# Kernel optimization log

Hardware: AMD Instinct MI355X
Metric: run time of the kernel (lower is better)

The kernel has to match this reference:

```python
import jax, jax.numpy as jnp
import numpy as np

N, E, P = 20000, 320000, 100000
TC, HID, H, OUT, PH = 256, 64, 4, 256, 512


def gat_conv(x, src, dst, n, W, a_src, a_dst, b):
    # PyG GATConv (eval, dropout=0): per-head linear, LeakyReLU(0.2) attention,
    # scatter-softmax over incoming edges, scatter-add aggregation, concat heads + bias.
    Hh, C = a_src.shape
    h = (x @ W).reshape(n, Hh, C)
    alpha_src = (h * a_src).sum(-1)  # [N, H]
    alpha_dst = (h * a_dst).sum(-1)  # [N, H]
    e = jax.nn.leaky_relu(alpha_src[src] + alpha_dst[dst], 0.2)  # [E, H]
    emax = jax.ops.segment_max(e, dst, num_segments=n)
    emax = jnp.where(jnp.isfinite(emax), emax, 0.0)
    p = jnp.exp(e - emax[dst])
    denom = jax.ops.segment_sum(p, dst, num_segments=n)
    alpha = p / jnp.maximum(denom[dst], 1e-16)  # [E, H]
    out = jax.ops.segment_sum(h[src] * alpha[:, :, None], dst, num_segments=n)  # [N, H, C]
    return out.reshape(n, Hh * C) + b


def setup_inputs() -> dict:
    key = jax.random.key(0)
    ks = jax.random.split(key, 24)
    s = 0.05
    inp = {
        "x": jax.random.normal(ks[0], (N, TC), jnp.float32),
        "edge_index": jax.random.randint(ks[1], (2, E), 0, N, jnp.int64),
        "u_nodes": jax.random.randint(ks[2], (P,), 0, N, jnp.int64),
        "v_nodes": jax.random.randint(ks[3], (P,), 0, N, jnp.int64),
        # GATConv 1: in=TC, out=HID per head, heads=H, concat
        "W1": jax.random.normal(ks[4], (TC, H * HID), jnp.float32) * s,
        "a1s": jax.random.normal(ks[5], (H, HID), jnp.float32) * s,
        "a1d": jax.random.normal(ks[6], (H, HID), jnp.float32) * s,
        "b1": jax.random.normal(ks[7], (H * HID,), jnp.float32) * s,
        # GATConv 2: in=H*HID, out=OUT, heads=1
        "W2": jax.random.normal(ks[8], (H * HID, OUT), jnp.float32) * s,
        "a2s": jax.random.normal(ks[9], (1, OUT), jnp.float32) * s,
        "a2d": jax.random.normal(ks[10], (1, OUT), jnp.float32) * s,
        "b2": jax.random.normal(ks[11], (OUT,), jnp.float32) * s,
        # gate MLP: (TC+OUT) -> (TC+OUT)//2 -> 1, Sigmoid
        "gw1": jax.random.normal(ks[12], (TC + OUT, (TC + OUT) // 2), jnp.float32) * s,
        "gb1": jax.random.normal(ks[13], ((TC + OUT) // 2,), jnp.float32) * s,
        "gw2": jax.random.normal(ks[14], ((TC + OUT) // 2, 1), jnp.float32) * s,
        "gb2": jax.random.normal(ks[15], (1,), jnp.float32) * s,
        # predictor: 2*OUT -> PH -> 1 (dropout is identity in eval)
        "pw1": jax.random.normal(ks[16], (2 * OUT, PH), jnp.float32) * s,
        "pb1": jax.random.normal(ks[17], (PH,), jnp.float32) * s,
        "pw2": jax.random.normal(ks[18], (PH, 1), jnp.float32) * s,
        "pb2": jax.random.normal(ks[19], (1,), jnp.float32) * s,
    }
    return inp


def reference(x, edge_index, u_nodes, v_nodes, W1, a1s, a1d, b1, W2, a2s, a2d, b2,
              gw1, gb1, gw2, gb2, pw1, pb1, pw2, pb2):
    n = x.shape[0]
    loops = jnp.arange(n, dtype=edge_index.dtype)
    src = jnp.concatenate([edge_index[0], loops])  # PyG GATConv adds self-loops
    dst = jnp.concatenate([edge_index[1], loops])
    h = jax.nn.elu(gat_conv(x, src, dst, n, W1, a1s, a1d, b1))
    h_graph = gat_conv(h, src, dst, n, W2, a2s, a2d, b2)
    gate_in = jnp.concatenate([x, h_graph], axis=-1)
    g = jax.nn.sigmoid(jax.nn.relu(gate_in @ gw1 + gb1) @ gw2 + gb2)  # [N,1]
    h_final = (1.0 - g) * x + g * h_graph
    pair = jnp.concatenate([h_final[u_nodes], h_final[v_nodes]], axis=-1)  # [P, 2*OUT]
    out = jax.nn.relu(pair @ pw1 + pb1) @ pw2 + pb2
    return out.squeeze(-1)
```

## Files before the change

### kernel.cpp

```cpp
#include <hip/hip_runtime.h>
#include <math.h>

#define N_NODES 20000
#define N_EDGES 320000
#define EPRIME  (N_EDGES + N_NODES)
#define NP      100000

typedef __bf16 bf16x8 __attribute__((ext_vector_type(8)));
typedef float  f32x4  __attribute__((ext_vector_type(4)));

__device__ __forceinline__ float b2f(unsigned short u) {
    union { float f; unsigned int v; } x; x.v = ((unsigned int)u) << 16; return x.f;
}
__device__ __forceinline__ unsigned short f2b(float f) {
    union { float f; unsigned int v; } x; x.f = f;
    unsigned int r = (x.v + 0x7fffu + ((x.v >> 16) & 1u)) >> 16;
    return (unsigned short)r;
}
__device__ __forceinline__ float lrelu02(float v) { return v > 0.0f ? v : 0.2f * v; }

__device__ __forceinline__ void gload16(const void* g, void* l) {
    __builtin_amdgcn_global_load_lds(
        (const __attribute__((address_space(1))) void*)g,
        (__attribute__((address_space(3))) void*)l, 16, 0, 0);
}

template<int ASRC, int EPI>
__global__ __launch_bounds__(256) void mgemm_k(
    const unsigned short* __restrict__ A0, const unsigned short* __restrict__ A1,
    const int* __restrict__ idxU, const int* __restrict__ idxV,
    const unsigned short* __restrict__ BT,
    const float* __restrict__ bias, const float* __restrict__ w2,
    unsigned short* __restrict__ Cb, float* __restrict__ outp,
    int M, int K, int Nn)
{
    __shared__ unsigned short As[2][4096];
    __shared__ unsigned short Bs[2][4096];

    const int tid = threadIdx.x;
    const int wave = tid >> 6, lane = tid & 63;
    const int row0 = blockIdx.x * 128, col0 = blockIdx.y * 128;
    const int ksub = (((lane & 3) ^ ((lane >> 3) & 3)) * 8);

    const unsigned short* aL[2];
    const unsigned short* aH[2];
    const unsigned short* bP[2];
    #pragma unroll
    for (int j = 0; j < 2; ++j) {
        const int r = j * 64 + wave * 16 + (lane >> 2);
        int ar = row0 + r; if (ar > M - 1) ar = M - 1;
        if (ASRC == 0)      { aL[j] = A0 + (long)ar * K;  aH[j] = aL[j]; }
        else if (ASRC == 1) { aL[j] = A0 + (long)ar * 256; aH[j] = A1 + (long)ar * 256; }
        else { const int u = idxU[ar], v = idxV[ar];
               aL[j] = A0 + (long)u * 256;  aH[j] = A0 + (long)v * 256; }
        bP[j] = BT + (long)(col0 + r) * K;
    }

    const int wm = wave >> 1, wn = wave & 1;
    const int lrow = lane & 15;
    const int lks = ((((lane >> 4) ^ ((lane >> 1) & 3)) & 3) * 8);

    f32x4 acc[4][4] = {};

    const int nT = K >> 5;
    int buf = 0;

    auto stage = [&](int bi, int t) {
        const int k0 = t << 5;
        #pragma unroll
        for (int j = 0; j < 2; ++j) {
            const unsigned short* ga;
            if (ASRC == 0) ga = aL[j] + k0 + ksub;
            else ga = (k0 < 256) ? (aL[j] + k0 + ksub) : (aH[j] + (k0 - 256) + ksub);
            const int ci = j * 256 + wave * 64 + lane;
            gload16(ga, &As[bi][ci * 8]);
            gload16(bP[j] + k0 + ksub, &Bs[bi][ci * 8]);
        }
    };

    stage(0, 0);
    __syncthreads();
    for (int t = 0; t < nT; ++t) {
        if (t + 1 < nT) stage(buf ^ 1, t + 1);
        bf16x8 a[4], b[4];
        #pragma unroll
        for (int i = 0; i < 4; ++i)
            a[i] = *(const bf16x8*)&As[buf][(wm * 64 + i * 16 + lrow) * 32 + lks];
        #pragma unroll
        for (int j = 0; j < 4; ++j)
            b[j] = *(const bf16x8*)&Bs[buf][(wn * 64 + j * 16 + lrow) * 32 + lks];
        #pragma unroll
        for (int i = 0; i < 4; ++i)
            #pragma unroll
            for (int j = 0; j < 4; ++j)
                acc[i][j] = __builtin_amdgcn_mfma_f32_16x16x32_bf16(a[i], b[j], acc[i][j], 0, 0, 0);
        __syncthreads();
        buf ^= 1;
    }

    if constexpr (EPI == 0 || EPI == 1) {
        #pragma unroll
        for (int i = 0; i < 4; ++i) {
            #pragma unroll
            for (int p = 0; p < 4; ++p) {
                const int row = row0 + wm * 64 + i * 16 + (lane >> 4) * 4 + p;
                if (row < M) {
                    #pragma unroll
                    for (int j = 0; j < 4; ++j) {
                        const int col = col0 + wn * 64 + j * 16 + (lane & 15);
                        float v = acc[i][j][p];
                        if (EPI == 1) { v += bias[col]; v = v > 0.f ? v : 0.f; }
                        Cb[(long)row * Nn + col] = f2b(v);
                    }
                }
            }
        }
    } else {
        float s[4][4];
        #pragma unroll
        for (int i = 0; i < 4; ++i) {
            #pragma unroll
            for (int p = 0; p < 4; ++p) {
                float t = 0.f;
                #pragma unroll
                for (int j = 0; j < 4; ++j) {
                    const int col = col0 + wn * 64 + j * 16 + (lane & 15);
                    float v = acc[i][j][p] + bias[col];
                    v = v > 0.f ? v : 0.f;
                    t += v * w2[col];
                }
                s[i][p] = t;
            }
        }
        #pragma unroll
        for (int off = 1; off < 16; off <<= 1) {
            #pragma unroll
            for (int i = 0; i < 4; ++i)
                #pragma unroll
                for (int p = 0; p < 4; ++p)
                    s[i][p] += __shfl_xor(s[i][p], off);
        }
        if ((lane & 15) == 0) {
            #pragma unroll
            for (int i = 0; i < 4; ++i)
                #pragma unroll
                for (int p = 0; p < 4; ++p) {
                    const int row = row0 + wm * 64 + i * 16 + (lane >> 4) * 4 + p;
                    if (row < M) atomicAdd(outp + row, s[i][p]);
                }
        }
    }
}

__global__ __launch_bounds__(256) void pair_k(
    const unsigned short* __restrict__ Z, const int* __restrict__ un,
    const int* __restrict__ vn, const float* __restrict__ pb1,
    const float* __restrict__ pw2, const float* __restrict__ pb2,
    float* __restrict__ out)
{
    const int wv = threadIdx.x >> 6, lane = threadIdx.x & 63;
    const int p = blockIdx.x * 4 + wv;
    if (p >= NP) return;
    const int u = un[p], v = vn[p];
    const int c0 = lane * 8;
    const uint4 zu = *(const uint4*)&Z[(long)u * 1024 + c0];
    const uint4 zv = *(const uint4*)&Z[(long)v * 1024 + 512 + c0];
    const float4 b1a = *(const float4*)&pb1[c0];
    const float4 b1b = *(const float4*)&pb1[c0 + 4];
    const float4 w2a = *(const float4*)&pw2[c0];
    const float4 w2b = *(const float4*)&pw2[c0 + 4];

    float zt[8], zb[8];
    zt[0] = b2f(zu.x & 0xffff); zt[1] = b2f(zu.x >> 16);
    zt[2] = b2f(zu.y & 0xffff); zt[3] = b2f(zu.y >> 16);
    zt[4] = b2f(zu.z & 0xffff); zt[5] = b2f(zu.z >> 16);
    zt[6] = b2f(zu.w & 0xffff); zt[7] = b2f(zu.w >> 16);
    zb[0] = b2f(zv.x & 0xffff); zb[1] = b2f(zv.x >> 16);
    zb[2] = b2f(zv.y & 0xffff); zb[3] = b2f(zv.y >> 16);
    zb[4] = b2f(zv.z & 0xffff); zb[5] = b2f(zv.z >> 16);
    zb[6] = b2f(zv.w & 0xffff); zb[7] = b2f(zv.w >> 16);

    const float bb[8] = {b1a.x, b1a.y, b1a.z, b1a.w, b1b.x, b1b.y, b1b.z, b1b.w};
    const float ww[8] = {w2a.x, w2a.y, w2a.z, w2a.w, w2b.x, w2b.y, w2b.z, w2b.w};
    float s = 0.f;
    #pragma unroll
    for (int q = 0; q < 8; ++q) {
        float t = zt[q] + zb[q] + bb[q];
        t = t > 0.f ? t : 0.f;
        s = fmaf(t, ww[q], s);
    }
    #pragma unroll
    for (int off = 1; off < 64; off <<= 1) s += __shfl_xor(s, off);
    if (lane == 0) out[p] = s + pb2[0];
}

__global__ __launch_bounds__(256) void castx_k(const float* __restrict__ x,
                                               unsigned short* __restrict__ xb)
{
    const int id = blockIdx.x * 256 + threadIdx.x;
    const float4 v = ((const float4*)x)[id];
    ushort4 o;
    o.x = f2b(v.x); o.y = f2b(v.y); o.z = f2b(v.z); o.w = f2b(v.w);
    ((ushort4*)xb)[id] = o;
}

__global__ __launch_bounds__(256) void tr_k(const float* __restrict__ B,
                                            unsigned short* __restrict__ BT,
                                            int K, int N)
{
    const int id = blockIdx.x * 256 + threadIdx.x;
    const int k = id / N, n = id % N;
    BT[(long)n * K + k] = f2b(B[id]);
}

__global__ __launch_bounds__(256) void tr2_k(const float* __restrict__ pw1,
                                             unsigned short* __restrict__ BT2)
{
    const int id = blockIdx.x * 256 + threadIdx.x;
    const int r = id >> 9, c = id & 511;
    const int j = (r < 256) ? c : (512 + c);
    const int k = (r < 256) ? r : (r - 256);
    BT2[j * 256 + k] = f2b(pw1[id]);
}

__global__ __launch_bounds__(256) void alpha1_k(
    const unsigned short* __restrict__ h1, const float* __restrict__ a1s,
    const float* __restrict__ a1d, float* __restrict__ as1, float* __restrict__ ad1)
{
    const int wid = threadIdx.x >> 6;
    const int lane = threadIdx.x & 63;
    const int n = blockIdx.x * 4 + wid;
    if (n >= N_NODES) return;
    float ps[4], pd[4];
    #pragma unroll
    for (int h = 0; h < 4; ++h) {
        const float hv = b2f(h1[(long)n * 256 + h * 64 + lane]);
        ps[h] = hv * a1s[h * 64 + lane];
        pd[h] = hv * a1d[h * 64 + lane];
    }
    #pragma unroll
    for (int off = 32; off > 0; off >>= 1) {
        #pragma unroll
        for (int h = 0; h < 4; ++h) {
            ps[h] += __shfl_xor(ps[h], off);
            pd[h] += __shfl_xor(pd[h], off);
        }
    }
    if (lane == 0) {
        #pragma unroll
        for (int h = 0; h < 4; ++h) {
            as1[n * 4 + h] = ps[h];
            ad1[n * 4 + h] = pd[h];
        }
    }
}

__global__ __launch_bounds__(256) void alpha2_k(
    const unsigned short* __restrict__ h2, const float* __restrict__ a2s,
    const float* __restrict__ a2d, float* __restrict__ as2, float* __restrict__ ad2)
{
    const int wid = threadIdx.x >> 6;
    const int lane = threadIdx.x & 63;
    const int n = blockIdx.x * 4 + wid;
    if (n >= N_NODES) return;
    float ps = 0.f, pd = 0.f;
    #pragma unroll
    for (int q = 0; q < 4; ++q) {
        const float hv = b2f(h2[(long)n * 256 + q * 64 + lane]);
        ps += hv * a2s[q * 64 + lane];
        pd += hv * a2d[q * 64 + lane];
    }
    #pragma unroll
    for (int off = 32; off > 0; off >>= 1) {
        ps += __shfl_xor(ps, off);
        pd += __shfl_xor(pd, off);
    }
    if (lane == 0) { as2[n] = ps; ad2[n] = pd; }
}

__global__ __launch_bounds__(256) void deg_init_k(int* __restrict__ deg)
{
    const int i = blockIdx.x * 256 + threadIdx.x;
    if (i < N_NODES) deg[i] = 1;
}

__global__ __launch_bounds__(256) void deg_count_k(const int* __restrict__ ei, int* __restrict__ deg)
{
    const int e = blockIdx.x * 256 + threadIdx.x;
    if (e < N_EDGES) atomicAdd(&deg[ei[N_EDGES + e]], 1);
}

__global__ __launch_bounds__(1024) void scan_k(const int* __restrict__ deg,
                                               int* __restrict__ indptr,
                                               int* __restrict__ pos)
{
    __shared__ int sums[1024];
    const int tid = threadIdx.x;
    const int CH = 20;
    const int start = tid * CH;
    const int end = min(start + CH, N_NODES);
    int s = 0;
    for (int i = start; i < end; ++i) s += deg[i];
    sums[tid] = s;
    __syncthreads();
    for (int off = 1; off < 1024; off <<= 1) {
        const int v = sums[tid];
        const int add = (tid >= off) ? sums[tid - off] : 0;
        __syncthreads();
        sums[tid] = v + add;
        __syncthreads();
    }
    int pre = sums[tid] - s;
    for (int i = start; i < end; ++i) {
        indptr[i] = pre;
        pos[i] = pre;
        pre += deg[i];
    }
    if (tid == 1023) indptr[N_NODES] = sums[1023];
}

__global__ __launch_bounds__(256) void fill_k(const int* __restrict__ ei,
                                              int* __restrict__ pos, int* __restrict__ csr)
{
    const int i = blockIdx.x * 256 + threadIdx.x;
    if (i < N_EDGES) {
        const int s = ei[i], d = ei[N_EDGES + i];
        const int p = atomicAdd(&pos[d], 1);
        csr[p] = s;
    } else if (i < EPRIME) {
        const int n = i - N_EDGES;
        const int p = atomicAdd(&pos[n], 1);
        csr[p] = n;
    }
}

__global__ __launch_bounds__(256) void agg1_k(
    const unsigned short* __restrict__ h1, const float* __restrict__ as1,
    const float* __restrict__ ad1, const int* __restrict__ indptr,
    const int* __restrict__ csr, const float* __restrict__ b1,
    unsigned short* __restrict__ out)
{
    __shared__ int   ssrc[4][64];
    __shared__ float sp[4][64 * 4];
    const int wv = threadIdx.x >> 6, lane = threadIdx.x & 63;
    const int n = blockIdx.x * 4 + wv;
    if (n >= N_NODES) return;

    const int beg = indptr[n], end = indptr[n + 1];
    const float4 ad = ((const float4*)ad1)[n];
    const int c0 = lane * 4;
    const int hd = lane >> 4;

    float acc[4] = {0.f, 0.f, 0.f, 0.f};
    float psum[4] = {0.f, 0.f, 0.f, 0.f};

    for (int base = beg; base < end; base += 64) {
        const int cnt = min(64, end - base);
        if (lane < cnt) {
            const int s = csr[base + lane];
            const float4 av = ((const float4*)as1)[s];
            float4 p;
            p.x = __expf(lrelu02(av.x + ad.x));
            p.y = __expf(lrelu02(av.y + ad.y));
            p.z = __expf(lrelu02(av.z + ad.z));
            p.w = __expf(lrelu02(av.w + ad.w));
            ssrc[wv][lane] = s;
            *(float4*)&sp[wv][lane * 4] = p;
            psum[0] += p.x; psum[1] += p.y; psum[2] += p.z; psum[3] += p.w;
        }
        asm volatile("s_waitcnt lgkmcnt(0)" ::: "memory");
        __builtin_amdgcn_sched_barrier(0);
        for (int e = 0; e < cnt; ++e) {
            const int s = ssrc[wv][e];
            const float w = sp[wv][e * 4 + hd];
            const ushort4 hv = *(const ushort4*)&h1[(long)s * 256 + c0];
            acc[0] = fmaf(w, b2f(hv.x), acc[0]);
            acc[1] = fmaf(w, b2f(hv.y), acc[1]);
            acc[2] = fmaf(w, b2f(hv.z), acc[2]);
            acc[3] = fmaf(w, b2f(hv.w), acc[3]);
        }
        __builtin_amdgcn_sched_barrier(0);
        __builtin_amdgcn_wave_barrier();
    }

    #pragma unroll
    for (int off = 1; off < 64; off <<= 1) {
        #pragma unroll
        for (int h = 0; h < 4; ++h) psum[h] += __shfl_xor(psum[h], off);
    }
    const float invd = 1.0f / psum[hd];

    ushort4 o;
    float v;
    v = acc[0] * invd + b1[c0 + 0]; o.x = f2b(v > 0.f ? v : (__expf(v) - 1.0f));
    v = acc[1] * invd + b1[c0 + 1]; o.y = f2b(v > 0.f ? v : (__expf(v) - 1.0f));
    v = acc[2] * invd + b1[c0 + 2]; o.z = f2b(v > 0.f ? v : (__expf(v) - 1.0f));
    v = acc[3] * invd + b1[c0 + 3]; o.w = f2b(v > 0.f ? v : (__expf(v) - 1.0f));
    *(ushort4*)&out[(long)n * 256 + c0] = o;
}

__global__ __launch_bounds__(256) void agg2_k(
    const unsigned short* __restrict__ h2, const float* __restrict__ as2,
    const float* __restrict__ ad2, const int* __restrict__ indptr,
    const int* __restrict__ csr, const float* __restrict__ b2,
    unsigned short* __restrict__ outb)
{
    __shared__ int   ssrc[4][64];
    __shared__ float sp[4][64];
    const int wv = threadIdx.x >> 6, lane = threadIdx.x & 63;
    const int n = blockIdx.x * 4 + wv;
    if (n >= N_NODES) return;

    const int beg = indptr[n], end = indptr[n + 1];
    const float adv = ad2[n];
    const int c0 = lane * 4;

    float acc[4] = {0.f, 0.f, 0.f, 0.f};
    float psum = 0.f;

    for (int base = beg; base < end; base += 64) {
        const int cnt = min(64, end - base);
        if (lane < cnt) {
            const int s = csr[base + lane];
            const float p = __expf(lrelu02(as2[s] + adv));
            ssrc[wv][lane] = s;
            sp[wv][lane] = p;
            psum += p;
        }
        asm volatile("s_waitcnt lgkmcnt(0)" ::: "memory");
        __builtin_amdgcn_sched_barrier(0);
        for (int e = 0; e < cnt; ++e) {
            const int s = ssrc[wv][e];
            const float w = sp[wv][e];
            const ushort4 hv = *(const ushort4*)&h2[(long)s * 256 + c0];
            acc[0] = fmaf(w, b2f(hv.x), acc[0]);
            acc[1] = fmaf(w, b2f(hv.y), acc[1]);
            acc[2] = fmaf(w, b2f(hv.z), acc[2]);
            acc[3] = fmaf(w, b2f(hv.w), acc[3]);
        }
        __builtin_amdgcn_sched_barrier(0);
        __builtin_amdgcn_wave_barrier();
    }

    #pragma unroll
    for (int off = 1; off < 64; off <<= 1) psum += __shfl_xor(psum, off);
    const float invd = 1.0f / psum;

    ushort4 o;
    o.x = f2b(acc[0] * invd + b2[c0 + 0]);
    o.y = f2b(acc[1] * invd + b2[c0 + 1]);
    o.z = f2b(acc[2] * invd + b2[c0 + 2]);
    o.w = f2b(acc[3] * invd + b2[c0 + 3]);
    *(ushort4*)&outb[(long)n * 256 + c0] = o;
}

__global__ __launch_bounds__(256) void gatefin_k(
    const unsigned short* __restrict__ ghid, const float* __restrict__ gw2,
    const float* __restrict__ gb2, const float* __restrict__ x,
    const unsigned short* __restrict__ hgb, unsigned short* __restrict__ hfb)
{
    const int wid = threadIdx.x >> 6;
    const int lane = threadIdx.x & 63;
    const int n = blockIdx.x * 4 + wid;
    if (n >= N_NODES) return;
    float s = 0.f;
    #pragma unroll
    for (int q = 0; q < 4; ++q)
        s += b2f(ghid[(long)n * 256 + q * 64 + lane]) * gw2[q * 64 + lane];
    #pragma unroll
    for (int off = 32; off > 0; off >>= 1) s += __shfl_xor(s, off);
    const float g = 1.0f / (1.0f + __expf(-(s + gb2[0])));
    #pragma unroll
    for (int q = 0; q < 4; ++q) {
        const int c = q * 64 + lane;
        const float xv = x[(long)n * 256 + c];
        const float hv = b2f(hgb[(long)n * 256 + c]);
        hfb[(long)n * 256 + c] = f2b((1.0f - g) * xv + g * hv);
    }
}

__global__ __launch_bounds__(256) void outinit_k(float* __restrict__ out, const float* __restrict__ pb2)
{
    const int p = blockIdx.x * 256 + threadIdx.x;
    if (p < NP) out[p] = pb2[0];
}

extern "C" void kernel_launch(void* const* d_in, const int* in_sizes, int n_in,
                              void* d_out, int out_size, void* d_ws, size_t ws_size,
                              hipStream_t stream)
{
    const float* x   = (const float*)d_in[0];
    const int*   ei  = (const int*)d_in[1];
    const int*   un  = (const int*)d_in[2];
    const int*   vn  = (const int*)d_in[3];
    const float* W1  = (const float*)d_in[4];
    const float* a1s = (const float*)d_in[5];
    const float* a1d = (const float*)d_in[6];
    const float* b1  = (const float*)d_in[7];
    const float* W2  = (const float*)d_in[8];
    const float* a2s = (const float*)d_in[9];
    const float* a2d = (const float*)d_in[10];
    const float* b2  = (const float*)d_in[11];
    const float* gw1 = (const float*)d_in[12];
    const float* gb1 = (const float*)d_in[13];
    const float* gw2 = (const float*)d_in[14];
    const float* gb2 = (const float*)d_in[15];
    const float* pw1 = (const float*)d_in[16];
    const float* pb1 = (const float*)d_in[17];
    const float* pw2 = (const float*)d_in[18];
    const float* pb2 = (const float*)d_in[19];
    float* out = (float*)d_out;

    dim3 b256(256);

    if (ws_size >= 58720256u) {
        unsigned short* Z     = (unsigned short*)d_ws;
        unsigned short* bufHb = Z;
        unsigned short* hgb   = Z + 5120000;
        unsigned short* xb    = Z + 10240000;
        unsigned short* hfb   = Z + 20480000;
        unsigned short* W1t   = hfb + 5120000;
        unsigned short* W2t   = W1t + 65536;
        unsigned short* gw1t  = W2t + 65536;
        unsigned short* pw1t2 = gw1t + 131072;
        float* as1v = (float*)(pw1t2 + 262144);
        float* ad1v = as1v + 80000;
        float* as2v = ad1v + 80000;
        float* ad2v = as2v + 20000;
        int* deg    = (int*)(ad2v + 20000);
        int* indptr = deg + 20000;
        int* pos    = indptr + 20032;
        int* csr    = pos + 20000;

        castx_k<<<5000, b256, 0, stream>>>(x, xb);
        tr_k<<<65536 / 256, b256, 0, stream>>>(W1, W1t, 256, 256);
        tr_k<<<65536 / 256, b256, 0, stream>>>(W2, W2t, 256, 256);
        tr_k<<<131072 / 256, b256, 0, stream>>>(gw1, gw1t, 512, 256);
        tr2_k<<<262144 / 256, b256, 0, stream>>>(pw1, pw1t2);
        deg_init_k<<<(N_NODES + 255) / 256, b256, 0, stream>>>(deg);
        deg_count_k<<<(N_EDGES + 255) / 256, b256, 0, stream>>>(ei, deg);
        scan_k<<<1, 1024, 0, stream>>>(deg, indptr, pos);
        fill_k<<<(EPRIME + 255) / 256, b256, 0, stream>>>(ei, pos, csr);

        mgemm_k<0, 0><<<dim3(157, 2), b256, 0, stream>>>(
            xb, nullptr, nullptr, nullptr, W1t, nullptr, nullptr, bufHb, nullptr,
            N_NODES, 256, 256);
        alpha1_k<<<5000, b256, 0, stream>>>(bufHb, a1s, a1d, as1v, ad1v);
        agg1_k<<<5000, b256, 0, stream>>>(bufHb, as1v, ad1v, indptr, csr, b1, hfb);

        mgemm_k<0, 0><<<dim3(157, 2), b256, 0, stream>>>(
            hfb, nullptr, nullptr, nullptr, W2t, nullptr, nullptr, bufHb, nullptr,
            N_NODES, 256, 256);
        alpha2_k<<<5000, b256, 0, stream>>>(bufHb, a2s, a2d, as2v, ad2v);
        agg2_k<<<5000, b256, 0, stream>>>(bufHb, as2v, ad2v, indptr, csr, b2, hgb);

        mgemm_k<1, 1><<<dim3(157, 2), b256, 0, stream>>>(
            xb, hgb, nullptr, nullptr, gw1t, gb1, nullptr, bufHb, nullptr,
            N_NODES, 512, 256);
        gatefin_k<<<5000, b256, 0, stream>>>(bufHb, gw2, gb2, x, hgb, hfb);

        mgemm_k<0, 0><<<dim3(157, 8), b256, 0, stream>>>(
            hfb, nullptr, nullptr, nullptr, pw1t2, nullptr, nullptr, Z, nullptr,
            N_NODES, 256, 1024);

        pair_k<<<25000, b256, 0, stream>>>(Z, un, vn, pb1, pw2, pb2, out);
        return;
    }

    unsigned short* bufHb = (unsigned short*)d_ws;
    unsigned short* h1ab  = bufHb + 5120000;
    unsigned short* hgb   = h1ab + 5120000;
    unsigned short* xb    = hgb + 5120000;
    unsigned short* W1t   = xb + 5120000;
    unsigned short* W2t   = W1t + 65536;
    unsigned short* gw1t  = W2t + 65536;
    unsigned short* pw1t  = gw1t + 131072;
    float* as1v = (float*)(pw1t + 262144);
    float* ad1v = as1v + 80000;
    float* as2v = ad1v + 80000;
    float* ad2v = as2v + 20000;
    int* deg    = (int*)(ad2v + 20000);
    int* indptr = deg + 20000;
    int* pos    = indptr + 20032;
    int* csr    = pos + 20000;
    if (ws_size < 46u * 1024u * 1024u) return;

    castx_k<<<5000, b256, 0, stream>>>(x, xb);
    tr_k<<<65536 / 256, b256, 0, stream>>>(W1, W1t, 256, 256);
    tr_k<<<65536 / 256, b256, 0, stream>>>(W2, W2t, 256, 256);
    tr_k<<<131072 / 256, b256, 0, stream>>>(gw1, gw1t, 512, 256);
    tr_k<<<262144 / 256, b256, 0, stream>>>(pw1, pw1t, 512, 512);
    deg_init_k<<<(N_NODES + 255) / 256, b256, 0, stream>>>(deg);
    deg_count_k<<<(N_EDGES + 255) / 256, b256, 0, stream>>>(ei, deg);
    scan_k<<<1, 1024, 0, stream>>>(deg, indptr, pos);
    fill_k<<<(EPRIME + 255) / 256, b256, 0, stream>>>(ei, pos, csr);

    mgemm_k<0, 0><<<dim3(157, 2), b256, 0, stream>>>(
        xb, nullptr, nullptr, nullptr, W1t, nullptr, nullptr, bufHb, nullptr,
        N_NODES, 256, 256);
    alpha1_k<<<5000, b256, 0, stream>>>(bufHb, a1s, a1d, as1v, ad1v);
    agg1_k<<<5000, b256, 0, stream>>>(bufHb, as1v, ad1v, indptr, csr, b1, h1ab);

    mgemm_k<0, 0><<<dim3(157, 2), b256, 0, stream>>>(
        h1ab, nullptr, nullptr, nullptr, W2t, nullptr, nullptr, bufHb, nullptr,
        N_NODES, 256, 256);
    alpha2_k<<<5000, b256, 0, stream>>>(bufHb, a2s, a2d, as2v, ad2v);
    agg2_k<<<5000, b256, 0, stream>>>(bufHb, as2v, ad2v, indptr, csr, b2, hgb);

    mgemm_k<1, 1><<<dim3(157, 2), b256, 0, stream>>>(
        xb, hgb, nullptr, nullptr, gw1t, gb1, nullptr, bufHb, nullptr,
        N_NODES, 512, 256);
    gatefin_k<<<5000, b256, 0, stream>>>(bufHb, gw2, gb2, x, hgb, h1ab);

    outinit_k<<<(NP + 255) / 256, b256, 0, stream>>>(out, pb2);
    mgemm_k<2, 2><<<dim3(782, 4), b256, 0, stream>>>(
        h1ab, nullptr, un, vn, pw1t, pb1, pw2, nullptr, out,
        NP, 512, 512);
}
```

Before: 264.1 us.

## Merge prep kernels, shrink GEMM row tiles, fuse gate MLP output into GEMM epilogue

Replaces the cast, transpose and init launches with one combined prep kernel. Adds a BM template parameter so the N=20000 GEMMs use 64-row tiles, giving more blocks to fill the CUs. The gate MLP's second layer and sigmoid input are folded into the GEMM epilogue through atomic row reductions, which removes the bf16 hidden-buffer round trip. The predictor's first-layer bias is added in the Z GEMM epilogue instead of in pair_k. Smaller tiles reload B more often, and the atomics add contention.

New measurement: 257.1 us. -2.7%, faster.

```diff
diff --git a/kernel.cpp b/kernel.cpp
--- a/kernel.cpp
+++ b/kernel.cpp
@@ -25,7 +25,7 @@
         (__attribute__((address_space(3))) void*)l, 16, 0, 0);
 }
 
-template<int ASRC, int EPI>
+template<int BM, int ASRC, int EPI>
 __global__ __launch_bounds__(256) void mgemm_k(
     const unsigned short* __restrict__ A0, const unsigned short* __restrict__ A1,
     const int* __restrict__ idxU, const int* __restrict__ idxV,
@@ -34,25 +34,33 @@
     unsigned short* __restrict__ Cb, float* __restrict__ outp,
     int M, int K, int Nn)
 {
-    __shared__ unsigned short As[2][4096];
+    constexpr int NJA   = BM / 64;
+    constexpr int MF    = BM / 32;
+    constexpr int WROWS = BM / 2;
+
+    __shared__ unsigned short As[2][BM * 32];
     __shared__ unsigned short Bs[2][4096];
 
     const int tid = threadIdx.x;
     const int wave = tid >> 6, lane = tid & 63;
-    const int row0 = blockIdx.x * 128, col0 = blockIdx.y * 128;
+    const int row0 = blockIdx.x * BM, col0 = blockIdx.y * 128;
     const int ksub = (((lane & 3) ^ ((lane >> 3) & 3)) * 8);
 
-    const unsigned short* aL[2];
-    const unsigned short* aH[2];
+    const unsigned short* aL[NJA];
+    const unsigned short* aH[NJA];
     const unsigned short* bP[2];
     #pragma unroll
-    for (int j = 0; j < 2; ++j) {
+    for (int j = 0; j < NJA; ++j) {
         const int r = j * 64 + wave * 16 + (lane >> 2);
         int ar = row0 + r; if (ar > M - 1) ar = M - 1;
         if (ASRC == 0)      { aL[j] = A0 + (long)ar * K;  aH[j] = aL[j]; }
         else if (ASRC == 1) { aL[j] = A0 + (long)ar * 256; aH[j] = A1 + (long)ar * 256; }
         else { const int u = idxU[ar], v = idxV[ar];
                aL[j] = A0 + (long)u * 256;  aH[j] = A0 + (long)v * 256; }
+    }
+    #pragma unroll
+    for (int j = 0; j < 2; ++j) {
+        const int r = j * 64 + wave * 16 + (lane >> 2);
         bP[j] = BT + (long)(col0 + r) * K;
     }
 
@@ -60,7 +68,7 @@
     const int lrow = lane & 15;
     const int lks = ((((lane >> 4) ^ ((lane >> 1) & 3)) & 3) * 8);
 
-    f32x4 acc[4][4] = {};
+    f32x4 acc[MF][4] = {};
 
     const int nT = K >> 5;
     int buf = 0;
@@ -68,12 +76,16 @@
     auto stage = [&](int bi, int t) {
         const int k0 = t << 5;
         #pragma unroll
-        for (int j = 0; j < 2; ++j) {
+        for (int j = 0; j < NJA; ++j) {
             const unsigned short* ga;
             if (ASRC == 0) ga = aL[j] + k0 + ksub;
             else ga = (k0 < 256) ? (aL[j] + k0 + ksub) : (aH[j] + (k0 - 256) + ksub);
             const int ci = j * 256 + wave * 64 + lane;
             gload16(ga, &As[bi][ci * 8]);
+        }
+        #pragma unroll
+        for (int j = 0; j < 2; ++j) {
+            const int ci = j * 256 + wave * 64 + lane;
             gload16(bP[j] + k0 + ksub, &Bs[bi][ci * 8]);
         }
     };
@@ -82,15 +94,15 @@
     __syncthreads();
     for (int t = 0; t < nT; ++t) {
         if (t + 1 < nT) stage(buf ^ 1, t + 1);
-        bf16x8 a[4], b[4];
-        #pragma unroll
-        for (int i = 0; i < 4; ++i)
-            a[i] = *(const bf16x8*)&As[buf][(wm * 64 + i * 16 + lrow) * 32 + lks];
+        bf16x8 a[MF], b[4];
+        #pragma unroll
+        for (int i = 0; i < MF; ++i)
+            a[i] = *(const bf16x8*)&As[buf][(wm * WROWS + i * 16 + lrow) * 32 + lks];
         #pragma unroll
         for (int j = 0; j < 4; ++j)
             b[j] = *(const bf16x8*)&Bs[buf][(wn * 64 + j * 16 + lrow) * 32 + lks];
         #pragma unroll
-        for (int i = 0; i < 4; ++i)
+        for (int i = 0; i < MF; ++i)
             #pragma unroll
             for (int j = 0; j < 4; ++j)
                 acc[i][j] = __builtin_amdgcn_mfma_f32_16x16x32_bf16(a[i], b[j], acc[i][j], 0, 0, 0);
@@ -98,27 +110,28 @@
         buf ^= 1;
     }
 
-    if constexpr (EPI == 0 || EPI == 1) {
-        #pragma unroll
-        for (int i = 0; i < 4; ++i) {
+    if constexpr (EPI == 0 || EPI == 1 || EPI == 3) {
+        #pragma unroll
+        for (int i = 0; i < MF; ++i) {
             #pragma unroll
             for (int p = 0; p < 4; ++p) {
-                const int row = row0 + wm * 64 + i * 16 + (lane >> 4) * 4 + p;
+                const int row = row0 + wm * WROWS + i * 16 + (lane >> 4) * 4 + p;
                 if (row < M) {
                     #pragma unroll
                     for (int j = 0; j < 4; ++j) {
                         const int col = col0 + wn * 64 + j * 16 + (lane & 15);
                         float v = acc[i][j][p];
                         if (EPI == 1) { v += bias[col]; v = v > 0.f ? v : 0.f; }
+                        if (EPI == 3) { if (col < 512) v += bias[col]; }
                         Cb[(long)row * Nn + col] = f2b(v);
                     }
                 }
             }
         }
     } else {
-        float s[4][4];
-        #pragma unroll
-        for (int i = 0; i < 4; ++i) {
+        float s[MF][4];
+        #pragma unroll
+        for (int i = 0; i < MF; ++i) {
             #pragma unroll
             for (int p = 0; p < 4; ++p) {
                 float t = 0.f;
@@ -135,17 +148,17 @@
         #pragma unroll
         for (int off = 1; off < 16; off <<= 1) {
             #pragma unroll
-            for (int i = 0; i < 4; ++i)
+            for (int i = 0; i < MF; ++i)
                 #pragma unroll
                 for (int p = 0; p < 4; ++p)
                     s[i][p] += __shfl_xor(s[i][p], off);
         }
         if ((lane & 15) == 0) {
             #pragma unroll
-            for (int i = 0; i < 4; ++i)
+            for (int i = 0; i < MF; ++i)
                 #pragma unroll
                 for (int p = 0; p < 4; ++p) {
-                    const int row = row0 + wm * 64 + i * 16 + (lane >> 4) * 4 + p;
+                    const int row = row0 + wm * WROWS + i * 16 + (lane >> 4) * 4 + p;
                     if (row < M) atomicAdd(outp + row, s[i][p]);
                 }
         }
@@ -154,9 +167,8 @@
 
 __global__ __launch_bounds__(256) void pair_k(
     const unsigned short* __restrict__ Z, const int* __restrict__ un,
-    const int* __restrict__ vn, const float* __restrict__ pb1,
-    const float* __restrict__ pw2, const float* __restrict__ pb2,
-    float* __restrict__ out)
+    const int* __restrict__ vn, const float* __restrict__ pw2,
+    const float* __restrict__ pb2, float* __restrict__ out)
 {
     const int wv = threadIdx.x >> 6, lane = threadIdx.x & 63;
     const int p = blockIdx.x * 4 + wv;
@@ -165,8 +177,6 @@
     const int c0 = lane * 8;
     const uint4 zu = *(const uint4*)&Z[(long)u * 1024 + c0];
     const uint4 zv = *(const uint4*)&Z[(long)v * 1024 + 512 + c0];
-    const float4 b1a = *(const float4*)&pb1[c0];
-    const float4 b1b = *(const float4*)&pb1[c0 + 4];
     const float4 w2a = *(const float4*)&pw2[c0];
     const float4 w2b = *(const float4*)&pw2[c0 + 4];
 
@@ -180,18 +190,56 @@
     zb[4] = b2f(zv.z & 0xffff); zb[5] = b2f(zv.z >> 16);
     zb[6] = b2f(zv.w & 0xffff); zb[7] = b2f(zv.w >> 16);
 
-    const float bb[8] = {b1a.x, b1a.y, b1a.z, b1a.w, b1b.x, b1b.y, b1b.z, b1b.w};
     const float ww[8] = {w2a.x, w2a.y, w2a.z, w2a.w, w2b.x, w2b.y, w2b.z, w2b.w};
     float s = 0.f;
     #pragma unroll
     for (int q = 0; q < 8; ++q) {
-        float t = zt[q] + zb[q] + bb[q];
+        float t = zt[q] + zb[q];
         t = t > 0.f ? t : 0.f;
         s = fmaf(t, ww[q], s);
     }
     #pragma unroll
     for (int off = 1; off < 64; off <<= 1) s += __shfl_xor(s, off);
     if (lane == 0) out[p] = s + pb2[0];
+}
+
+__global__ __launch_bounds__(256) void prep_k(
+    const float* __restrict__ x, unsigned short* __restrict__ xb,
+    const float* __restrict__ W1, unsigned short* __restrict__ W1t,
+    const float* __restrict__ W2, unsigned short* __restrict__ W2t,
+    const float* __restrict__ gw1, unsigned short* __restrict__ gw1t,
+    const float* __restrict__ pw1, unsigned short* __restrict__ pw1t2,
+    int* __restrict__ deg, float* __restrict__ gacc)
+{
+    const int bid = blockIdx.x, tid = threadIdx.x;
+    if (bid < 5000) {
+        const int id = bid * 256 + tid;
+        const float4 v = ((const float4*)x)[id];
+        ushort4 o;
+        o.x = f2b(v.x); o.y = f2b(v.y); o.z = f2b(v.z); o.w = f2b(v.w);
+        ((ushort4*)xb)[id] = o;
+    } else if (bid < 5256) {
+        const int id = (bid - 5000) * 256 + tid;
+        W1t[(id & 255) * 256 + (id >> 8)] = f2b(W1[id]);
+    } else if (bid < 5512) {
+        const int id = (bid - 5256) * 256 + tid;
+        W2t[(id & 255) * 256 + (id >> 8)] = f2b(W2[id]);
+    } else if (bid < 6024) {
+        const int id = (bid - 5512) * 256 + tid;
+        gw1t[(id & 255) * 512 + (id >> 8)] = f2b(gw1[id]);
+    } else if (bid < 7048) {
+        const int id = (bid - 6024) * 256 + tid;
+        const int r = id >> 9, c = id & 511;
+        const int j = (r < 256) ? c : (512 + c);
+        const int k = (r < 256) ? r : (r - 256);
+        pw1t2[j * 256 + k] = f2b(pw1[id]);
+    } else if (bid < 7127) {
+        const int i = (bid - 7048) * 256 + tid;
+        if (i < N_NODES) deg[i] = 1;
+    } else {
+        const int i = (bid - 7127) * 256 + tid;
+        if (i < N_NODES) gacc[i] = 0.f;
+    }
 }
 
 __global__ __launch_bounds__(256) void castx_k(const float* __restrict__ x,
@@ -211,16 +259,6 @@
     const int id = blockIdx.x * 256 + threadIdx.x;
     const int k = id / N, n = id % N;
     BT[(long)n * K + k] = f2b(B[id]);
-}
-
-__global__ __launch_bounds__(256) void tr2_k(const float* __restrict__ pw1,
-                                             unsigned short* __restrict__ BT2)
-{
-    const int id = blockIdx.x * 256 + threadIdx.x;
-    const int r = id >> 9, c = id & 511;
-    const int j = (r < 256) ? c : (512 + c);
-    const int k = (r < 256) ? r : (r - 256);
-    BT2[j * 256 + k] = f2b(pw1[id]);
 }
 
 __global__ __launch_bounds__(256) void alpha1_k(
@@ -454,6 +492,25 @@
     *(ushort4*)&outb[(long)n * 256 + c0] = o;
 }
 
+__global__ __launch_bounds__(256) void gatefin2_k(
+    const float* __restrict__ gacc, const float* __restrict__ gb2,
+    const float* __restrict__ x, const unsigned short* __restrict__ hgb,
+    unsigned short* __restrict__ hfb)
+{
+    const int wid = threadIdx.x >> 6;
+    const int lane = threadIdx.x & 63;
+    const int n = blockIdx.x * 4 + wid;
+    if (n >= N_NODES) return;
+    const float g = 1.0f / (1.0f + __expf(-(gacc[n] + gb2[0])));
+    #pragma unroll
+    for (int q = 0; q < 4; ++q) {
+        const int c = q * 64 + lane;
+        const float xv = x[(long)n * 256 + c];
+        const float hv = b2f(hgb[(long)n * 256 + c]);
+        hfb[(long)n * 256 + c] = f2b((1.0f - g) * xv + g * hv);
+    }
+}
+
 __global__ __launch_bounds__(256) void gatefin_k(
     const unsigned short* __restrict__ ghid, const float* __restrict__ gw2,
     const float* __restrict__ gb2, const float* __restrict__ x,
@@ -483,6 +540,16 @@
 {
     const int p = blockIdx.x * 256 + threadIdx.x;
     if (p < NP) out[p] = pb2[0];
+}
+
+__global__ __launch_bounds__(256) void tr2_k(const float* __restrict__ pw1,
+                                             unsigned short* __restrict__ BT2)
+{
+    const int id = blockIdx.x * 256 + threadIdx.x;
+    const int r = id >> 9, c = id & 511;
+    const int j = (r < 256) ? c : (512 + c);
+    const int k = (r < 256) ? r : (r - 256);
+    BT2[j * 256 + k] = f2b(pw1[id]);
 }
 
 extern "C" void kernel_launch(void* const* d_in, const int* in_sizes, int n_in,
@@ -531,39 +598,36 @@
         int* indptr = deg + 20000;
         int* pos    = indptr + 20032;
         int* csr    = pos + 20000;
-
-        castx_k<<<5000, b256, 0, stream>>>(x, xb);
-        tr_k<<<65536 / 256, b256, 0, stream>>>(W1, W1t, 256, 256);
-        tr_k<<<65536 / 256, b256, 0, stream>>>(W2, W2t, 256, 256);
-        tr_k<<<131072 / 256, b256, 0, stream>>>(gw1, gw1t, 512, 256);
-        tr2_k<<<262144 / 256, b256, 0, stream>>>(pw1, pw1t2);
-        deg_init_k<<<(N_NODES + 255) / 256, b256, 0, stream>>>(deg);
+        float* gacc = (float*)(csr + EPRIME);
+
+        prep_k<<<7206, b256, 0, stream>>>(x, xb, W1, W1t, W2, W2t, gw1, gw1t,
+                                          pw1, pw1t2, deg, gacc);
         deg_count_k<<<(N_EDGES + 255) / 256, b256, 0, stream>>>(ei, deg);
         scan_k<<<1, 1024, 0, stream>>>(deg, indptr, pos);
         fill_k<<<(EPRIME + 255) / 256, b256, 0, stream>>>(ei, pos, csr);
 
-        mgemm_k<0, 0><<<dim3(157, 2), b256, 0, stream>>>(
+        mgemm_k<64, 0, 0><<<dim3(313, 2), b256, 0, stream>>>(
             xb, nullptr, nullptr, nullptr, W1t, nullptr, nullptr, bufHb, nullptr,
             N_NODES, 256, 256);
         alpha1_k<<<5000, b256, 0, stream>>>(bufHb, a1s, a1d, as1v, ad1v);
         agg1_k<<<5000, b256, 0, stream>>>(bufHb, as1v, ad1v, indptr, csr, b1, hfb);
 
-        mgemm_k<0, 0><<<dim3(157, 2), b256, 0, stream>>>(
+        mgemm_k<64, 0, 0><<<dim3(313, 2), b256, 0, stream>>>(
             hfb, nullptr, nullptr, nullptr, W2t, nullptr, nullptr, bufHb, nullptr,
             N_NODES, 256, 256);
         alpha2_k<<<5000, b256, 0, stream>>>(bufHb, a2s, a2d, as2v, ad2v);
         agg2_k<<<5000, b256, 0, stream>>>(bufHb, as2v, ad2v, indptr, csr, b2, hgb);
 
-        mgemm_k<1, 1><<<dim3(157, 2), b256, 0, stream>>>(
-            xb, hgb, nullptr, nullptr, gw1t, gb1, nullptr, bufHb, nullptr,
+        mgemm_k<64, 1, 2><<<dim3(313, 2), b256, 0, stream>>>(
+            xb, hgb, nullptr, nullptr, gw1t, gb1, gw2, nullptr, gacc,
             N_NODES, 512, 256);
-        gatefin_k<<<5000, b256, 0, stream>>>(bufHb, gw2, gb2, x, hgb, hfb);
-
-        mgemm_k<0, 0><<<dim3(157, 8), b256, 0, stream>>>(
-            hfb, nullptr, nullptr, nullptr, pw1t2, nullptr, nullptr, Z, nullptr,
+        gatefin2_k<<<5000, b256, 0, stream>>>(gacc, gb2, x, hgb, hfb);
+
+        mgemm_k<128, 0, 3><<<dim3(157, 8), b256, 0, stream>>>(
+            hfb, nullptr, nullptr, nullptr, pw1t2, pb1, nullptr, Z, nullptr,
             N_NODES, 256, 1024);
 
-        pair_k<<<25000, b256, 0, stream>>>(Z, un, vn, pb1, pw2, pb2, out);
+        pair_k<<<25000, b256, 0, stream>>>(Z, un, vn, pw2, pb2, out);
         return;
     }
 
@@ -595,25 +659,25 @@
     scan_k<<<1, 1024, 0, stream>>>(deg, indptr, pos);
     fill_k<<<(EPRIME + 255) / 256, b256, 0, stream>>>(ei, pos, csr);
 
-    mgemm_k<0, 0><<<dim3(157, 2), b256, 0, stream>>>(
+    mgemm_k<128, 0, 0><<<dim3(157, 2), b256, 0, stream>>>(
         xb, nullptr, nullptr, nullptr, W1t, nullptr, nullptr, bufHb, nullptr,
         N_NODES, 256, 256);
     alpha1_k<<<5000, b256, 0, stream>>>(bufHb, a1s, a1d, as1v, ad1v);
     agg1_k<<<5000, b256, 0, stream>>>(bufHb, as1v, ad1v, indptr, csr, b1, h1ab);
 
-    mgemm_k<0, 0><<<dim3(157, 2), b256, 0, stream>>>(
+    mgemm_k<128, 0, 0><<<dim3(157, 2), b256, 0, stream>>>(
         h1ab, nullptr, nullptr, nullptr, W2t, nullptr, nullptr, bufHb, nullptr,
         N_NODES, 256, 256);
     alpha2_k<<<5000, b256, 0, stream>>>(bufHb, a2s, a2d, as2v, ad2v);
     agg2_k<<<5000, b256, 0, stream>>>(bufHb, as2v, ad2v, indptr, csr, b2, hgb);
 
-    mgemm_k<1, 1><<<dim3(157, 2), b256, 0, stream>>>(
+    mgemm_k<128, 1, 1><<<dim3(157, 2), b256, 0, stream>>>(
         xb, hgb, nullptr, nullptr, gw1t, gb1, nullptr, bufHb, nullptr,
         N_NODES, 512, 256);
     gatefin_k<<<5000, b256, 0, stream>>>(bufHb, gw2, gb2, x, hgb, h1ab);
 
     outinit_k<<<(NP + 255) / 256, b256, 0, stream>>>(out, pb2);
-    mgemm_k<2, 2><<<dim3(782, 4), b256, 0, stream>>>(
+    mgemm_k<128, 2, 2><<<dim3(782, 4), b256, 0, stream>>>(
         h1ab, nullptr, un, vn, pw1t, pb1, pw2, nullptr, out,
         NP, 512, 512);
 }
```
